# Kernel tuning notes

Hardware: AMD Instinct MI355X
Metric: run time of the kernel (lower is better)

The kernel has to match this reference:

```python
import jax, jax.numpy as jnp
import numpy as np

# init_kwargs constants
K = 512            # out_channels (k)
THRESH = 10.0
KWTA = 16
INHIBITION_RADIUS = 0   # output spatial is 1x1; radius>0 would zero all features after 1st winner
RF_SIZE = 50
LENGTH = 2000
TIMESTEPS = 32
IN_CHANNELS = 1


def setup_inputs() -> dict:
    key = jax.random.key(0)
    k1, k2 = jax.random.split(key)
    rec_field = jax.random.normal(k1, (TIMESTEPS, IN_CHANNELS, RF_SIZE, LENGTH), dtype=jnp.float32)
    # LocalConvolution with kernel_size == input_size -> single output position;
    # weight is effectively (K, C, rf_size, length)
    weight = jax.random.normal(k2, (K, IN_CHANNELS, RF_SIZE, LENGTH), dtype=jnp.float32) * 0.02
    return {"rec_field": rec_field, "weight": weight}


def _forward(rec_field, weight):
    T = rec_field.shape[0]
    # local conv collapses to a per-timestep dense projection: (T, K)
    out = jnp.einsum('tchw,kchw->tk', rec_field, weight)
    # sf.fire: threshold potentials (keep > THRESH), spikes = sign
    pot = jnp.where(out > THRESH, out, jnp.zeros((), out.dtype))
    spike = jnp.sign(pot)
    # sf.get_k_winners (spatial dims are 1x1, work on (K,))
    nspk = spike.sum(axis=0)                                   # (K,) number of spiking timesteps
    first = jnp.clip((T - nspk).astype(jnp.int32), 0, T - 1)   # index of first spike
    values = jnp.take_along_axis(pot, first[None, :], axis=0)[0]  # potential at first spike, (K,)
    v = jnp.max(values * jnp.sign(nspk)) * T                   # large additive constant
    total = nspk * values + nspk * v                           # == truncated_pot.sum(dim=0)

    def step(tot, _):
        i = jnp.argmax(tot)
        valid = tot[i] != 0
        tot = jnp.where(valid, tot.at[i].set(0.0), tot)        # suppress winning feature
        # columnar spatial inhibition is a no-op here: output spatial size is 1x1, radius=0
        return tot, jnp.where(valid, i, -1)

    _, winners = jax.lax.scan(step, total, None, length=KWTA)  # (KWTA,) feature indices or -1
    coef = jnp.zeros((pot.shape[1],), pot.dtype).at[jnp.clip(winners, 0, None)].max(
        jnp.where(winners >= 0, 1.0, 0.0))
    # torch.mul(pot, coef).sign() ; restore (T, K, 1, 1) layout
    return jnp.sign(pot * coef[None, :])[:, :, None, None]


def reference(rec_field, weight):
    return _forward(rec_field, weight)
```

## Files before the change

kernel.cpp:

```cpp
#include <hip/hip_runtime.h>

#define RED    100000
#define TT     32
#define KF     512
#define THRESH 10.0f
#define KWTA   16

#define CHUNKS 125
#define CHUNK  800
#define RB     32
#define NSTAGE 25
#define TNK    64
#define NKT    8
#define KK     2

template <int ATOMIC>
__global__ __launch_bounds__(256, 2)
void gemm_k(const float* __restrict__ rec, const float* __restrict__ wgt,
            float* __restrict__ dst) {
  __shared__ float Al[TT][RB];

  const int chunk = blockIdx.x;
  const int kt    = blockIdx.y;
  const int tid   = threadIdx.x;
  const int kg    = tid >> 3;
  const int slot  = tid & 7;

  const float* ap = rec + (size_t)kg * RED + chunk * CHUNK + slot * 4;
  const float* bp = wgt + (size_t)(kt * TNK + kg) * RED + chunk * CHUNK + slot * 4;
  const size_t bstride = (size_t)32 * RED;

  float acc[TT][KK];
#pragma unroll
  for (int t = 0; t < TT; ++t) { acc[t][0] = 0.f; acc[t][1] = 0.f; }

  float4 av = *(const float4*)ap;
  float4 b0 = *(const float4*)bp;
  float4 b1 = *(const float4*)(bp + bstride);

#pragma unroll 1
  for (int s = 0; s < NSTAGE; ++s) {
    __syncthreads();
    *(float4*)&Al[kg][slot * 4] = av;
    __syncthreads();
    const float4 cb0 = b0, cb1 = b1;
    if (s + 1 < NSTAGE) {
      ap += RB; bp += RB;
      av = *(const float4*)ap;
      b0 = *(const float4*)bp;
      b1 = *(const float4*)(bp + bstride);
    }
#pragma unroll
    for (int t = 0; t < TT; ++t) {
      const float4 a = *(const float4*)&Al[t][slot * 4];
      acc[t][0] = fmaf(a.x, cb0.x, acc[t][0]);
      acc[t][0] = fmaf(a.y, cb0.y, acc[t][0]);
      acc[t][0] = fmaf(a.z, cb0.z, acc[t][0]);
      acc[t][0] = fmaf(a.w, cb0.w, acc[t][0]);
      acc[t][1] = fmaf(a.x, cb1.x, acc[t][1]);
      acc[t][1] = fmaf(a.y, cb1.y, acc[t][1]);
      acc[t][1] = fmaf(a.z, cb1.z, acc[t][1]);
      acc[t][1] = fmaf(a.w, cb1.w, acc[t][1]);
    }
  }

#pragma unroll
  for (int m = 1; m <= 4; m <<= 1) {
#pragma unroll
    for (int t = 0; t < TT; ++t) {
      acc[t][0] += __shfl_xor(acc[t][0], m, 64);
      acc[t][1] += __shfl_xor(acc[t][1], m, 64);
    }
  }

  if (ATOMIC) {
#pragma unroll
    for (int t = 0; t < TT; ++t) {
      if (slot == (t >> 2)) {
        atomicAdd(&dst[t * KF + kt * TNK + kg     ], acc[t][0]);
        atomicAdd(&dst[t * KF + kt * TNK + kg + 32], acc[t][1]);
      }
    }
  } else {
    float* p = dst + (size_t)(chunk * NKT + kt) * TT * TNK;
#pragma unroll
    for (int t = 0; t < TT; ++t) {
      if (slot == (t >> 2)) {
        p[t * TNK + kg     ] = acc[t][0];
        p[t * TNK + kg + 32] = acc[t][1];
      }
    }
  }
}

__global__ __launch_bounds__(256)
void reduce_k(const float* __restrict__ part, float* __restrict__ om) {
  const int i  = blockIdx.x * 256 + threadIdx.x;
  const int t  = i >> 9;
  const int k  = i & 511;
  const int kt = k >> 6;
  const int kk = k & 63;
  const float* p = part + (size_t)kt * TT * TNK + (size_t)t * TNK + kk;
  float s = 0.f;
#pragma unroll 5
  for (int c = 0; c < CHUNKS; ++c) s += p[(size_t)c * NKT * TT * TNK];
  om[i] = s;
}

__global__ __launch_bounds__(512)
void kwta_k(const float* __restrict__ om, float* __restrict__ out) {
  __shared__ float tot[KF];
  __shared__ float coef[KF];
  __shared__ float wmax[8];
  __shared__ int   widx[8];
  __shared__ float bflag;
  const int k    = threadIdx.x;
  const int lane = k & 63;
  const int wv   = k >> 6;

  int ns = 0;
#pragma unroll
  for (int t = 0; t < TT; ++t) ns += (om[t * KF + k] > THRESH) ? 1 : 0;
  int first = TT - ns;
  if (first > TT - 1) first = TT - 1;
  float pf = om[first * KF + k];
  pf = (pf > THRESH) ? pf : 0.0f;

  float m = (ns > 0) ? pf : 0.0f;
#pragma unroll
  for (int off = 1; off <= 32; off <<= 1) m = fmaxf(m, __shfl_xor(m, off, 64));
  if (lane == 0) wmax[wv] = m;
  __syncthreads();
  float v = wmax[0];
#pragma unroll
  for (int w = 1; w < 8; ++w) v = fmaxf(v, wmax[w]);
  v *= (float)TT;

  const float t1 = (float)ns * pf;
  const float t2 = (float)ns * v;
  tot[k]  = t1 + t2;
  coef[k] = 0.0f;
  __syncthreads();

  for (int it = 0; it < KWTA; ++it) {
    float val = tot[k];
    int   idx = k;
#pragma unroll
    for (int off = 1; off <= 32; off <<= 1) {
      const float ov = __shfl_xor(val, off, 64);
      const int   oi = __shfl_xor(idx, off, 64);
      if (ov > val || (ov == val && oi < idx)) { val = ov; idx = oi; }
    }
    if (lane == 0) { wmax[wv] = val; widx[wv] = idx; }
    __syncthreads();
    if (k == 0) {
      float bv = wmax[0]; int bi = widx[0];
#pragma unroll
      for (int w = 1; w < 8; ++w)
        if (wmax[w] > bv || (wmax[w] == bv && widx[w] < bi)) { bv = wmax[w]; bi = widx[w]; }
      if (bv != 0.0f) { tot[bi] = 0.0f; coef[bi] = 1.0f; bflag = 1.0f; }
      else            { bflag = 0.0f; }
    }
    __syncthreads();
    if (bflag == 0.0f) break;
  }
  __syncthreads();

  for (int i = k; i < TT * KF; i += KF) {
    const int kk = i & 511;
    const float p = om[i];
    out[i] = (p > THRESH && coef[kk] != 0.0f) ? 1.0f : 0.0f;
  }
}

extern "C" void kernel_launch(void* const* d_in, const int* in_sizes, int n_in,
                              void* d_out, int out_size, void* d_ws, size_t ws_size,
                              hipStream_t stream) {
  const float* rec = (const float*)d_in[0];
  const float* wgt = (const float*)d_in[1];
  float* out = (float*)d_out;
  float* om  = (float*)d_out;
  const size_t part_bytes = (size_t)CHUNKS * NKT * TT * TNK * sizeof(float);

  if (ws_size >= part_bytes) {
    float* part = (float*)d_ws;
    gemm_k<0><<<dim3(CHUNKS, NKT), 256, 0, stream>>>(rec, wgt, part);
    reduce_k<<<(TT * KF) / 256, 256, 0, stream>>>(part, om);
  } else {
    hipMemsetAsync(om, 0, (size_t)TT * KF * sizeof(float), stream);
    gemm_k<1><<<dim3(CHUNKS, NKT), 256, 0, stream>>>(rec, wgt, om);
  }
  kwta_k<<<1, 512, 0, stream>>>(om, out);
}
```

Measured before the change: 343.5 us.

## Widen per-thread K tile to four outputs and double-buffer the A tile in LDS

Each block now covers 128 output features instead of 64, with each thread accumulating four feature columns, so every A value loaded from LDS is reused across more FMAs. The grid shrinks from 8 to 4 K-tiles. The A tile in shared memory is double-buffered, which cuts the two barriers per stage down to one and lets the next stage's store overlap the current compute. The cost is more accumulator registers (128 floats) under launch_bounds(256,2), which risks spills or lower occupancy, and there are half as many blocks to spread across the CUs.

```diff
diff --git a/kernel.cpp b/kernel.cpp
--- a/kernel.cpp
+++ b/kernel.cpp
@@ -10,15 +10,15 @@
 #define CHUNK  800
 #define RB     32
 #define NSTAGE 25
-#define TNK    64
-#define NKT    8
-#define KK     2
+#define TNK    128
+#define NKT    4
+#define KK     4
 
 template <int ATOMIC>
 __global__ __launch_bounds__(256, 2)
 void gemm_k(const float* __restrict__ rec, const float* __restrict__ wgt,
             float* __restrict__ dst) {
-  __shared__ float Al[TT][RB];
+  __shared__ float Al[2][TT][RB];
 
   const int chunk = blockIdx.x;
   const int kt    = blockIdx.y;
@@ -28,31 +28,40 @@
 
   const float* ap = rec + (size_t)kg * RED + chunk * CHUNK + slot * 4;
   const float* bp = wgt + (size_t)(kt * TNK + kg) * RED + chunk * CHUNK + slot * 4;
-  const size_t bstride = (size_t)32 * RED;
+  const size_t bs = (size_t)32 * RED;
 
   float acc[TT][KK];
 #pragma unroll
-  for (int t = 0; t < TT; ++t) { acc[t][0] = 0.f; acc[t][1] = 0.f; }
+  for (int t = 0; t < TT; ++t)
+#pragma unroll
+    for (int c = 0; c < KK; ++c) acc[t][c] = 0.f;
 
   float4 av = *(const float4*)ap;
   float4 b0 = *(const float4*)bp;
-  float4 b1 = *(const float4*)(bp + bstride);
+  float4 b1 = *(const float4*)(bp + bs);
+  float4 b2 = *(const float4*)(bp + 2 * bs);
+  float4 b3 = *(const float4*)(bp + 3 * bs);
+  *(float4*)&Al[0][kg][slot * 4] = av;
+  ap += RB;
+  av = *(const float4*)ap;
+  __syncthreads();
 
 #pragma unroll 1
   for (int s = 0; s < NSTAGE; ++s) {
-    __syncthreads();
-    *(float4*)&Al[kg][slot * 4] = av;
-    __syncthreads();
-    const float4 cb0 = b0, cb1 = b1;
+    const int cur = s & 1;
+    const float4 cb0 = b0, cb1 = b1, cb2 = b2, cb3 = b3;
     if (s + 1 < NSTAGE) {
+      *(float4*)&Al[cur ^ 1][kg][slot * 4] = av;
       ap += RB; bp += RB;
       av = *(const float4*)ap;
       b0 = *(const float4*)bp;
-      b1 = *(const float4*)(bp + bstride);
+      b1 = *(const float4*)(bp + bs);
+      b2 = *(const float4*)(bp + 2 * bs);
+      b3 = *(const float4*)(bp + 3 * bs);
     }
 #pragma unroll
     for (int t = 0; t < TT; ++t) {
-      const float4 a = *(const float4*)&Al[t][slot * 4];
+      const float4 a = *(const float4*)&Al[cur][t][slot * 4];
       acc[t][0] = fmaf(a.x, cb0.x, acc[t][0]);
       acc[t][0] = fmaf(a.y, cb0.y, acc[t][0]);
       acc[t][0] = fmaf(a.z, cb0.z, acc[t][0]);
@@ -61,24 +70,34 @@
       acc[t][1] = fmaf(a.y, cb1.y, acc[t][1]);
       acc[t][1] = fmaf(a.z, cb1.z, acc[t][1]);
       acc[t][1] = fmaf(a.w, cb1.w, acc[t][1]);
-    }
+      acc[t][2] = fmaf(a.x, cb2.x, acc[t][2]);
+      acc[t][2] = fmaf(a.y, cb2.y, acc[t][2]);
+      acc[t][2] = fmaf(a.z, cb2.z, acc[t][2]);
+      acc[t][2] = fmaf(a.w, cb2.w, acc[t][2]);
+      acc[t][3] = fmaf(a.x, cb3.x, acc[t][3]);
+      acc[t][3] = fmaf(a.y, cb3.y, acc[t][3]);
+      acc[t][3] = fmaf(a.z, cb3.z, acc[t][3]);
+      acc[t][3] = fmaf(a.w, cb3.w, acc[t][3]);
+    }
+    __syncthreads();
   }
 
 #pragma unroll
   for (int m = 1; m <= 4; m <<= 1) {
 #pragma unroll
-    for (int t = 0; t < TT; ++t) {
-      acc[t][0] += __shfl_xor(acc[t][0], m, 64);
-      acc[t][1] += __shfl_xor(acc[t][1], m, 64);
-    }
+    for (int t = 0; t < TT; ++t)
+#pragma unroll
+      for (int c = 0; c < KK; ++c)
+        acc[t][c] += __shfl_xor(acc[t][c], m, 64);
   }
 
   if (ATOMIC) {
 #pragma unroll
     for (int t = 0; t < TT; ++t) {
       if (slot == (t >> 2)) {
-        atomicAdd(&dst[t * KF + kt * TNK + kg     ], acc[t][0]);
-        atomicAdd(&dst[t * KF + kt * TNK + kg + 32], acc[t][1]);
+#pragma unroll
+        for (int c = 0; c < KK; ++c)
+          atomicAdd(&dst[t * KF + kt * TNK + kg + 32 * c], acc[t][c]);
       }
     }
   } else {
@@ -86,8 +105,9 @@
 #pragma unroll
     for (int t = 0; t < TT; ++t) {
       if (slot == (t >> 2)) {
-        p[t * TNK + kg     ] = acc[t][0];
-        p[t * TNK + kg + 32] = acc[t][1];
+#pragma unroll
+        for (int c = 0; c < KK; ++c)
+          p[t * TNK + kg + 32 * c] = acc[t][c];
       }
     }
   }
@@ -98,8 +118,8 @@
   const int i  = blockIdx.x * 256 + threadIdx.x;
   const int t  = i >> 9;
   const int k  = i & 511;
-  const int kt = k >> 6;
-  const int kk = k & 63;
+  const int kt = k >> 7;
+  const int kk = k & 127;
   const float* p = part + (size_t)kt * TT * TNK + (size_t)t * TNK + kk;
   float s = 0.f;
 #pragma unroll 5
```

New measurement: 354.2 us. 1.03x slower.
